# Kernel optimization log

Hardware: AMD Instinct MI355X
Metric: run time of the kernel (lower is better)

The kernel has to match this reference:

```python
import jax, jax.numpy as jnp
import numpy as np

N = 8192      # num nodes (pad index == N, matching the original's 15004 sentinel)
IN = 128; H = 128; OUT = 128
T = 512       # number of teams
L = 30        # max_len
SAMPLE = 5    # sample team size
DCAT = 2 * H + OUT


def _glorot(k, shape):
    lim = np.sqrt(6.0 / (shape[0] + shape[1]))
    return jax.random.uniform(k, shape, jnp.float32, -lim, lim)


def setup_inputs() -> dict:
    key = jax.random.key(0)
    ks = jax.random.split(key, 32)
    x = jax.random.normal(ks[0], (1, N, IN), jnp.float32)
    # sparse-ish binary dense adjacency, avg degree ~16 (memory-bound adj@x)
    adj = (jax.random.uniform(ks[1], (1, N, N), jnp.float32) < 16.0 / N).astype(jnp.float32)
    # team index matrix, ragged lengths in [SAMPLE+1, L], padded with N
    lens = jax.random.randint(ks[2], (T,), SAMPLE + 1, L + 1)
    ids = jax.random.randint(ks[3], (T, L), 0, N)
    teams = jnp.where(jnp.arange(L)[None, :] < lens[:, None], ids, N)
    # DenseGraphConv params: lin_rel (W,b) on adj@x, lin_root (no bias) on x
    p = dict(
        W1r=_glorot(ks[4], (IN, H)), b1=jnp.zeros((H,), jnp.float32), W1s=_glorot(ks[5], (IN, H)),
        W2r=_glorot(ks[6], (H, H)), b2=jnp.zeros((H,), jnp.float32), W2s=_glorot(ks[7], (H, H)),
        W3r=_glorot(ks[8], (H, OUT)), b3=jnp.zeros((OUT,), jnp.float32), W3s=_glorot(ks[9], (H, OUT)),
        g1=jnp.ones((H,), jnp.float32), be1=jnp.zeros((H,), jnp.float32),
        g2=jnp.ones((H,), jnp.float32), be2=jnp.zeros((H,), jnp.float32),
        g3=jnp.ones((OUT,), jnp.float32), be3=jnp.zeros((OUT,), jnp.float32),
        Wl=_glorot(ks[10], (DCAT, OUT)), bl=jnp.zeros((OUT,), jnp.float32),
        att=_glorot(ks[11], (T, L)),  # xavier_uniform'd attention vectors
    )
    return dict(x=x, adj=adj, teams=teams, sample_len=SAMPLE, **p)


def _bn(h, g, b):
    # BatchNorm1d in training mode over flattened (B*N, C), biased variance
    B, n, C = h.shape
    h2 = h.reshape(-1, C)
    mu = h2.mean(0)
    var = h2.var(0)
    return (((h2 - mu) * jax.lax.rsqrt(var + 1e-5)) * g + b).reshape(B, n, C)


def _conv(x, adj, Wr, br, Ws):
    # DenseGraphConv: lin_rel(adj @ x) + lin_root(x)
    return jnp.einsum('bnm,bmf,fo->bno', adj, x, Wr) + br + jnp.einsum('bnf,fo->bno', x, Ws)


def reference(x, adj, teams, sample_len, W1r, b1, W1s, W2r, b2, W2s, W3r, b3, W3s,
              g1, be1, g2, be2, g3, be3, Wl, bl, att):
    x1 = _bn(jax.nn.relu(_conv(x, adj, W1r, b1, W1s)), g1, be1)
    x2 = _bn(jax.nn.relu(_conv(x1, adj, W2r, b2, W2s)), g2, be2)
    x3 = _bn(jax.nn.relu(_conv(x2, adj, W3r, b3, W3s)), g3, be3)
    xcat = jnp.concatenate([x1, x2, x3], axis=-1)               # [1,N,DCAT]
    s = jax.nn.relu(xcat @ Wl + bl)
    appended = jnp.concatenate([xcat[0], jnp.zeros((1, xcat.shape[-1]), xcat.dtype)], 0)  # [N+1,D]
    gathered = appended[teams]                                   # [T,L,D] ragged gather
    # team: full softmax over attention vector (pad positions keep softmax mass,
    # but gather the zero row -> contribute zero, matching the original)
    a_team = jax.nn.softmax(att, axis=-1)
    team_emb = jnp.einsum('tl,tld->td', a_team, gathered)
    pos = jnp.arange(teams.shape[1])[None, :]
    # sample: sub-softmax over the attention entries at the sample members' positions
    m_s = pos < sample_len
    a_s = jax.nn.softmax(jnp.where(m_s, att, -1e30), axis=-1)
    sample_emb = jnp.einsum('tl,tld->td', a_s, gathered)
    # remain: team minus sample minus pad sentinel
    m_r = (pos >= sample_len) & (teams != N)
    a_r = jax.nn.softmax(jnp.where(m_r, att, -1e30), axis=-1)
    remain_emb = jnp.einsum('tl,tld->td', a_r, gathered)
    return s, xcat, team_emb, sample_emb, remain_emb
```

## Files before the change

### kernel.cpp

```cpp
#include <hip/hip_runtime.h>
#include <stdint.h>

#define NN 8192
#define CC 128
#define TT 512
#define LL 30
#define CAP 64

typedef unsigned int uint32;
typedef unsigned short u16;

typedef float f32x4 __attribute__((ext_vector_type(4)));
typedef short bf16x8 __attribute__((ext_vector_type(8)));

__device__ __forceinline__ float bf2f(uint32 h) { return __uint_as_float(h << 16); }
__device__ __forceinline__ u16 f2bf(float f) {
    uint32 u = __float_as_uint(f);
    u = (u + 0x7fffu + ((u >> 16) & 1u)) >> 16;
    return (u16)u;
}
__device__ __forceinline__ uint32 pack2(float a, float b) {
    return (uint32)f2bf(a) | ((uint32)f2bf(b) << 16);
}

__device__ __forceinline__ void stats_reduce(const float* __restrict__ P,
                                             const float* __restrict__ g,
                                             const float* __restrict__ be,
                                             float* __restrict__ coefOut, int tid) {
    __shared__ float SS[256], QQ[256];
    int c = tid & 127, half = tid >> 7;
    float s = 0.f, q = 0.f;
    int b0 = half * 128;
#pragma unroll 8
    for (int b = b0; b < b0 + 128; ++b) {
        s += P[b * 256 + c];
        q += P[b * 256 + 128 + c];
    }
    SS[tid] = s; QQ[tid] = q;
    __syncthreads();
    if (tid < 128) {
        float sum = SS[tid] + SS[tid + 128];
        float sq = QQ[tid] + QQ[tid + 128];
        float mu = sum * (1.f / NN);
        float var = sq * (1.f / NN) - mu * mu;
        float rs = rsqrtf(var + 1e-5f);
        float a = g[tid] * rs;
        coefOut[tid] = a;
        coefOut[128 + tid] = be[tid] - mu * a;
    }
}

__global__ __launch_bounds__(256) void k_pre(
    const float* __restrict__ adj,
    const float* __restrict__ W1r, const float* __restrict__ W1s,
    const float* __restrict__ W2r, const float* __restrict__ W2s,
    const float* __restrict__ W3r, const float* __restrict__ W3s,
    const float* __restrict__ Wl, const float* __restrict__ x0,
    int* __restrict__ nbr, int* __restrict__ cnt,
    u16* __restrict__ wfrag, u16* __restrict__ x0bf,
    u16* __restrict__ yp1, u16* __restrict__ yp2, u16* __restrict__ yp3,
    u16* __restrict__ Abraw, float* __restrict__ coefs) {
    int b = blockIdx.x, tid = threadIdx.x;
    if (b < 2048) {
        int row = b * 4 + (tid >> 6);
        int lane = tid & 63;
        const float4* arow = (const float4*)(adj + (size_t)row * NN);
        int base = 0;
        int* dst = nbr + (size_t)row * CAP;
        for (int it = 0; it < 32; ++it) {
            float4 v = arow[it * 64 + lane];
            float vv[4] = {v.x, v.y, v.z, v.w};
#pragma unroll
            for (int j = 0; j < 4; ++j) {
                unsigned long long m = __ballot(vv[j] != 0.f);
                if (vv[j] != 0.f) {
                    int pos = base + __popcll(m & ((1ull << lane) - 1ull));
                    if (pos < CAP) dst[pos] = it * 256 + lane * 4 + j;
                }
                base += __popcll(m);
            }
        }
        int nn = base < CAP ? base : CAP;
        int npad = (nn + 3) & ~3;
        for (int p = nn + lane; p < npad; p += 64) dst[p] = NN;
        if (lane == 0) cnt[row] = nn;
        int c = lane * 2;
        float a0 = 0.f, a1 = 0.f;
        for (int j = 0; j < npad; j += 4) {
            int4 m = *(const int4*)(dst + j);
            if (m.x < NN) { float2 v = *(const float2*)(x0 + (size_t)m.x * CC + c); a0 += v.x; a1 += v.y; }
            if (m.y < NN) { float2 v = *(const float2*)(x0 + (size_t)m.y * CC + c); a0 += v.x; a1 += v.y; }
            if (m.z < NN) { float2 v = *(const float2*)(x0 + (size_t)m.z * CC + c); a0 += v.x; a1 += v.y; }
            if (m.w < NN) { float2 v = *(const float2*)(x0 + (size_t)m.w * CC + c); a0 += v.x; a1 += v.y; }
        }
        *(uint32*)(Abraw + (size_t)row * CC + c) = pack2(a0, a1);
    } else if (b < 2336) {
        int bb = b - 2048;
        const float* Wa;
        const float* Wb;
        int tile, gbase;
        if (bb < 64)       { Wa = W1r; Wb = W1s; tile = bb;       gbase = 0; }
        else if (bb < 128) { Wa = W2r; Wb = W2s; tile = bb - 64;  gbase = 64; }
        else if (bb < 192) { Wa = W3r; Wb = W3s; tile = bb - 128; gbase = 128; }
        else               { Wa = Wl;  Wb = nullptr; tile = bb - 192; gbase = 192; }
        int kt = tile >> 3, nt = tile & 7;
        int lane = tid & 63, i0 = (tid >> 6) * 2;
        int n = nt * 16 + (lane & 15);
        u16* dst = wfrag + ((size_t)(gbase + tile) * 64 + lane) * 8;
#pragma unroll
        for (int ii = 0; ii < 2; ++ii) {
            int i = i0 + ii;
            int k = kt * 32 + ((lane >> 4) * 8) + i;
            float v;
            if (Wb) v = (k < 128) ? Wa[k * CC + n] : Wb[(k - 128) * CC + n];
            else    v = Wa[k * CC + n];
            dst[i] = f2bf(v);
        }
    } else if (b < 3360) {
        int idx = (b - 2336) * 1024 + tid * 4;
        float4 v = *(const float4*)(x0 + idx);
        ushort4 o;
        o.x = f2bf(v.x); o.y = f2bf(v.y); o.z = f2bf(v.z); o.w = f2bf(v.w);
        *(ushort4*)(x0bf + idx) = o;
    } else {
        if (tid < 128) {
            x0bf[(size_t)NN * CC + tid] = 0;
            yp1[(size_t)NN * CC + tid] = 0;
            yp2[(size_t)NN * CC + tid] = 0;
            yp3[(size_t)NN * CC + tid] = 0;
            coefs[tid] = 1.f;
            coefs[128 + tid] = 0.f;
        }
    }
}

__global__ __launch_bounds__(256) void k_agg(const u16* __restrict__ src,
                                             const int* __restrict__ nbr,
                                             const int* __restrict__ cnt,
                                             u16* __restrict__ Abraw,
                                             const float* __restrict__ P,
                                             const float* __restrict__ g,
                                             const float* __restrict__ be,
                                             float* __restrict__ coefOut) {
    if (blockIdx.x >= 2048) {
        stats_reduce(P, g, be, coefOut, threadIdx.x);
        return;
    }
    int row = blockIdx.x * 4 + (threadIdx.x >> 6);
    int lane = threadIdx.x & 63;
    int c = lane * 2;
    int nreal = cnt[row];
    int npad = (nreal + 3) & ~3;
    const int* nb = nbr + (size_t)row * CAP;
    float a0 = 0.f, a1 = 0.f;
    for (int j = 0; j < npad; j += 4) {
        int4 m = *(const int4*)(nb + j);
        uint32 v0 = *(const uint32*)(src + (size_t)m.x * CC + c);
        uint32 v1 = *(const uint32*)(src + (size_t)m.y * CC + c);
        uint32 v2 = *(const uint32*)(src + (size_t)m.z * CC + c);
        uint32 v3 = *(const uint32*)(src + (size_t)m.w * CC + c);
        a0 += bf2f(v0 & 0xffffu); a1 += bf2f(v0 >> 16);
        a0 += bf2f(v1 & 0xffffu); a1 += bf2f(v1 >> 16);
        a0 += bf2f(v2 & 0xffffu); a1 += bf2f(v2 >> 16);
        a0 += bf2f(v3 & 0xffffu); a1 += bf2f(v3 >> 16);
    }
    *(uint32*)(Abraw + (size_t)row * CC + c) = pack2(a0, a1);
}

__global__ __launch_bounds__(512) void k_gemm(const u16* __restrict__ Abraw,
                                              const u16* __restrict__ yprev,
                                              const int* __restrict__ cnt,
                                              const u16* __restrict__ wfrag,
                                              const float* __restrict__ bias,
                                              const float* __restrict__ coefIn,
                                              u16* __restrict__ yp,
                                              float* __restrict__ partials) {
    __shared__ u16 A[32][264];
    __shared__ float sSum[CC], sSq[CC];
    int tid = threadIdx.x, lane = tid & 63, wid = tid >> 6;
    int row0 = blockIdx.x * 32;
    if (tid < CC) { sSum[tid] = 0.f; sSq[tid] = 0.f; }
    for (int i = tid; i < 1024; i += 512) {
        int r = i >> 5, k = (i & 31) * 8;
        int row = row0 + r;
        uint4 raw;
        float fn;
        int c;
        if (k < 128) {
            c = k;
            raw = *(const uint4*)(Abraw + (size_t)row * CC + k);
            fn = (float)cnt[row];
        } else {
            c = k - 128;
            raw = *(const uint4*)(yprev + (size_t)row * CC + c);
            fn = 1.f;
        }
        float4 a0 = *(const float4*)(coefIn + c);
        float4 a1 = *(const float4*)(coefIn + c + 4);
        float4 b0 = *(const float4*)(coefIn + 128 + c);
        float4 b1 = *(const float4*)(coefIn + 128 + c + 4);
        uint4 o;
        o.x = pack2(a0.x * bf2f(raw.x & 0xffffu) + b0.x * fn, a0.y * bf2f(raw.x >> 16) + b0.y * fn);
        o.y = pack2(a0.z * bf2f(raw.y & 0xffffu) + b0.z * fn, a0.w * bf2f(raw.y >> 16) + b0.w * fn);
        o.z = pack2(a1.x * bf2f(raw.z & 0xffffu) + b1.x * fn, a1.y * bf2f(raw.z >> 16) + b1.y * fn);
        o.w = pack2(a1.z * bf2f(raw.w & 0xffffu) + b1.z * fn, a1.w * bf2f(raw.w >> 16) + b1.w * fn);
        *(uint4*)&A[r][k] = o;
    }
    __syncthreads();

    int mh = wid >> 2, nh = wid & 3;
    int arow = mh * 16 + (lane & 15);
    int kg = (lane >> 4) * 8;
    f32x4 acc[2];
#pragma unroll
    for (int nt = 0; nt < 2; ++nt) acc[nt] = (f32x4){0.f, 0.f, 0.f, 0.f};
#pragma unroll
    for (int kt = 0; kt < 8; ++kt) {
        bf16x8 a = *(const bf16x8*)&A[arow][kt * 32 + kg];
        const u16* wb = wfrag + ((size_t)(kt * 8 + nh * 2) * 64 + lane) * 8;
#pragma unroll
        for (int nt = 0; nt < 2; ++nt) {
            bf16x8 bfr = *(const bf16x8*)(wb + (size_t)nt * 512);
            acc[nt] = __builtin_amdgcn_mfma_f32_16x16x32_bf16(a, bfr, acc[nt], 0, 0, 0);
        }
    }
    int rowb = row0 + mh * 16 + ((lane >> 4) * 4);
#pragma unroll
    for (int nt = 0; nt < 2; ++nt) {
        int col = nh * 32 + nt * 16 + (lane & 15);
        float bv = bias[col];
        float s1 = 0.f, s2 = 0.f;
#pragma unroll
        for (int q = 0; q < 4; ++q) {
            float y = acc[nt][q] + bv;
            y = y > 0.f ? y : 0.f;
            yp[(size_t)(rowb + q) * CC + col] = f2bf(y);
            s1 += y;
            s2 += y * y;
        }
        s1 += __shfl_xor(s1, 16); s1 += __shfl_xor(s1, 32);
        s2 += __shfl_xor(s2, 16); s2 += __shfl_xor(s2, 32);
        if ((lane >> 4) == 0) { atomicAdd(&sSum[col], s1); atomicAdd(&sSq[col], s2); }
    }
    __syncthreads();
    if (tid < CC) {
        partials[(size_t)blockIdx.x * 256 + tid] = sSum[tid];
        partials[(size_t)blockIdx.x * 256 + CC + tid] = sSq[tid];
    }
}

__global__ __launch_bounds__(256) void k_coef3(const float* __restrict__ P,
                                               const float* __restrict__ g,
                                               const float* __restrict__ be,
                                               float* __restrict__ coefOut) {
    stats_reduce(P, g, be, coefOut, threadIdx.x);
}

__global__ __launch_bounds__(256) void k_out(
    const u16* __restrict__ yp1, const u16* __restrict__ yp2, const u16* __restrict__ yp3,
    const float* __restrict__ coefs,
    const u16* __restrict__ wfrag, const float* __restrict__ bias,
    const int* __restrict__ teams, const int* __restrict__ slen_p,
    const float* __restrict__ att,
    float* __restrict__ sout, float* __restrict__ xcat,
    float* __restrict__ oT, float* __restrict__ oS, float* __restrict__ oR) {
    int b = blockIdx.x, tid = threadIdx.x;
    if (b < 512) {
        __shared__ u16 A[16][392];
        int lane = tid & 63, wid = tid >> 6;
        int row0 = b * 16;
        for (int i = tid; i < 768; i += 256) {
            int r = i / 48, kk = (i % 48) * 8;
            int seg = kk >> 7, c = kk & 127;
            const u16* sp = (seg == 0 ? yp1 : seg == 1 ? yp2 : yp3) + (size_t)(row0 + r) * CC + c;
            uint4 raw = *(const uint4*)sp;
            const float* cf = coefs + seg * 256;
            float4 av0 = *(const float4*)(cf + c);
            float4 av1 = *(const float4*)(cf + c + 4);
            float4 bv0 = *(const float4*)(cf + 128 + c);
            float4 bv1 = *(const float4*)(cf + 128 + c + 4);
            uint4 o;
            o.x = pack2(av0.x * bf2f(raw.x & 0xffffu) + bv0.x, av0.y * bf2f(raw.x >> 16) + bv0.y);
            o.y = pack2(av0.z * bf2f(raw.y & 0xffffu) + bv0.z, av0.w * bf2f(raw.y >> 16) + bv0.w);
            o.z = pack2(av1.x * bf2f(raw.z & 0xffffu) + bv1.x, av1.y * bf2f(raw.z >> 16) + bv1.y);
            o.w = pack2(av1.z * bf2f(raw.w & 0xffffu) + bv1.z, av1.w * bf2f(raw.w >> 16) + bv1.w);
            *(uint4*)&A[r][kk] = o;
        }
        __syncthreads();
        int nh = wid;
        int arow = lane & 15;
        int kg = (lane >> 4) * 8;
        f32x4 acc[2];
#pragma unroll
        for (int nt = 0; nt < 2; ++nt) acc[nt] = (f32x4){0.f, 0.f, 0.f, 0.f};
#pragma unroll
        for (int kt = 0; kt < 12; ++kt) {
            bf16x8 a = *(const bf16x8*)&A[arow][kt * 32 + kg];
            const u16* wb = wfrag + ((size_t)(kt * 8 + nh * 2) * 64 + lane) * 8;
#pragma unroll
            for (int nt = 0; nt < 2; ++nt) {
                bf16x8 bfr = *(const bf16x8*)(wb + (size_t)nt * 512);
                acc[nt] = __builtin_amdgcn_mfma_f32_16x16x32_bf16(a, bfr, acc[nt], 0, 0, 0);
            }
        }
        int rowb = row0 + ((lane >> 4) * 4);
#pragma unroll
        for (int nt = 0; nt < 2; ++nt) {
            int col = nh * 32 + nt * 16 + (lane & 15);
            float bv = bias[col];
#pragma unroll
            for (int q = 0; q < 4; ++q) {
                float y = acc[nt][q] + bv;
                sout[(size_t)(rowb + q) * CC + col] = y > 0.f ? y : 0.f;
            }
        }
    } else if (b < 1024) {
        __shared__ float wT[LL], wS[LL], wR[LL];
        __shared__ int ids[LL];
        int t = b - 512;
        if (tid < 64) {
            int lane = tid;
            bool act = lane < LL;
            float a = act ? att[t * LL + lane] : 0.f;
            int id = act ? teams[t * LL + lane] : NN;
            if (act) ids[lane] = id;
            int sl = *slen_p;
            const float NEG = -1e30f;
            float v = act ? a : NEG;
#pragma unroll
            for (int o = 32; o > 0; o >>= 1) v = fmaxf(v, __shfl_xor(v, o));
            float mT = v;
            float eT = act ? __expf(a - mT) : 0.f;
            v = eT;
#pragma unroll
            for (int o = 32; o > 0; o >>= 1) v += __shfl_xor(v, o);
            float sT = v;
            bool inS = act && (lane < sl);
            v = inS ? a : NEG;
#pragma unroll
            for (int o = 32; o > 0; o >>= 1) v = fmaxf(v, __shfl_xor(v, o));
            float mS = v;
            float eS = inS ? __expf(a - mS) : 0.f;
            v = eS;
#pragma unroll
            for (int o = 32; o > 0; o >>= 1) v += __shfl_xor(v, o);
            float sS = v;
            bool inR = act && (lane >= sl) && (id != NN);
            v = inR ? a : NEG;
#pragma unroll
            for (int o = 32; o > 0; o >>= 1) v = fmaxf(v, __shfl_xor(v, o));
            float mR = v;
            float eR = inR ? __expf(a - mR) : 0.f;
            v = eR;
#pragma unroll
            for (int o = 32; o > 0; o >>= 1) v += __shfl_xor(v, o);
            float sR = v;
            if (act) {
                wT[lane] = eT / sT;
                wS[lane] = eS / sS;
                wR[lane] = eR / sR;
            }
        }
        __syncthreads();
        for (int d = tid; d < 384; d += 256) {
            int seg = d >> 7, c = d & 127;
            const u16* xb = seg == 0 ? yp1 : seg == 1 ? yp2 : yp3;
            float ca = coefs[seg * 256 + c];
            float cb = coefs[seg * 256 + 128 + c];
            float aT = 0.f, aS = 0.f, aR = 0.f;
            for (int l = 0; l < LL; ++l) {
                int id = ids[l];
                if (id < NN) {
                    float vv = ca * bf2f((uint32)xb[(size_t)id * CC + c]) + cb;
                    aT += wT[l] * vv;
                    aS += wS[l] * vv;
                    aR += wR[l] * vv;
                }
            }
            oT[(size_t)t * 384 + d] = aT;
            oS[(size_t)t * 384 + d] = aS;
            oR[(size_t)t * 384 + d] = aR;
        }
    } else {
        int idx = (b - 1024) * 256 + tid;
        int n = idx / 96;
        int k = (idx % 96) * 4;
        int seg = k >> 7, c = k & 127;
        const u16* sp = (seg == 0 ? yp1 : seg == 1 ? yp2 : yp3) + (size_t)n * CC + c;
        ushort4 raw = *(const ushort4*)sp;
        const float* cf = coefs + seg * 256;
        float4 a = *(const float4*)(cf + c);
        float4 bb = *(const float4*)(cf + 128 + c);
        float4 o;
        o.x = a.x * bf2f((uint32)raw.x) + bb.x;
        o.y = a.y * bf2f((uint32)raw.y) + bb.y;
        o.z = a.z * bf2f((uint32)raw.z) + bb.z;
        o.w = a.w * bf2f((uint32)raw.w) + bb.w;
        *(float4*)(xcat + (size_t)n * 384 + k) = o;
    }
}

extern "C" void kernel_launch(void* const* d_in, const int* in_sizes, int n_in,
                              void* d_out, int out_size, void* d_ws, size_t ws_size,
                              hipStream_t stream) {
    const float* x = (const float*)d_in[0];
    const float* adj = (const float*)d_in[1];
    const int* teams = (const int*)d_in[2];
    const int* slen = (const int*)d_in[3];
    const float* W1r = (const float*)d_in[4];
    const float* b1 = (const float*)d_in[5];
    const float* W1s = (const float*)d_in[6];
    const float* W2r = (const float*)d_in[7];
    const float* b2 = (const float*)d_in[8];
    const float* W2s = (const float*)d_in[9];
    const float* W3r = (const float*)d_in[10];
    const float* b3 = (const float*)d_in[11];
    const float* W3s = (const float*)d_in[12];
    const float* g1 = (const float*)d_in[13];
    const float* be1 = (const float*)d_in[14];
    const float* g2 = (const float*)d_in[15];
    const float* be2 = (const float*)d_in[16];
    const float* g3 = (const float*)d_in[17];
    const float* be3 = (const float*)d_in[18];
    const float* Wl = (const float*)d_in[19];
    const float* bl = (const float*)d_in[20];
    const float* att = (const float*)d_in[21];

    float* out = (float*)d_out;
    float* s_out = out;
    float* xcat = out + (size_t)NN * CC;
    float* oT = xcat + (size_t)NN * 384;
    float* oS = oT + (size_t)TT * 384;
    float* oR = oS + (size_t)TT * 384;

    char* ws = (char*)d_ws;
    size_t off = 0;
    int* nbr = (int*)(ws + off); off += (size_t)NN * CAP * 4;
    int* cnt = (int*)(ws + off); off += (size_t)NN * 4;
    u16* x0bf = (u16*)(ws + off); off += (size_t)(NN + 1) * CC * 2;
    u16* yp1 = (u16*)(ws + off); off += (size_t)(NN + 1) * CC * 2;
    u16* yp2 = (u16*)(ws + off); off += (size_t)(NN + 1) * CC * 2;
    u16* yp3 = (u16*)(ws + off); off += (size_t)(NN + 1) * CC * 2;
    u16* Abraw = (u16*)(ws + off); off += (size_t)NN * CC * 2;
    u16* wfrag = (u16*)(ws + off); off += (size_t)288 * 512 * 2;
    float* partials = (float*)(ws + off); off += (size_t)256 * 256 * 4;
    float* coefs = (float*)(ws + off); off += (size_t)4 * 256 * 4;

    k_pre<<<3361, 256, 0, stream>>>(adj, W1r, W1s, W2r, W2s, W3r, W3s, Wl, x,
                                    nbr, cnt, wfrag, x0bf, yp1, yp2, yp3, Abraw, coefs);
    k_gemm<<<256, 512, 0, stream>>>(Abraw, x0bf, cnt, wfrag, b1, coefs, yp1, partials);
    k_agg<<<2049, 256, 0, stream>>>(yp1, nbr, cnt, Abraw, partials, g1, be1, coefs + 256);
    k_gemm<<<256, 512, 0, stream>>>(Abraw, yp1, cnt, wfrag + 64 * 512, b2, coefs + 256, yp2, partials);
    k_agg<<<2049, 256, 0, stream>>>(yp2, nbr, cnt, Abraw, partials, g2, be2, coefs + 512);
    k_gemm<<<256, 512, 0, stream>>>(Abraw, yp2, cnt, wfrag + 128 * 512, b3, coefs + 512, yp3, partials);
    k_coef3<<<1, 256, 0, stream>>>(partials, g3, be3, coefs + 768);
    k_out<<<4096, 256, 0, stream>>>(yp1, yp2, yp3, coefs + 256,
                                    wfrag + 192 * 512, bl, teams, slen, att,
                                    s_out, xcat, oT, oS, oR);
}
```

Baseline: 129.7 us.

## Accumulate BatchNorm stats with fixed-point atomics and drop separate reduce kernel

Each GEMM block now adds its per-column sum and sum-of-squares into a global 64-bit fixed-point accumulator with integer atomics. This replaces the per-block partials array and the extra reduction block in k_agg, and removes the separate k_coef3 launch. Consumer kernels (the next GEMM and k_out) recompute the BN scale and shift from the accumulated stats in shared memory. The layer-1 GEMM converts x to bf16 inline, so the x0bf conversion pass and its buffer are gone. The costs are atomic contention on 256 addresses, redundant coefficient recomputation in every k_out block, and fixed-point quantization of the stats.

Result: no change. 131.4 us (+1.3%).

```diff
diff --git a/kernel.cpp b/kernel.cpp
--- a/kernel.cpp
+++ b/kernel.cpp
@@ -8,10 +8,14 @@
 #define CAP 64
 
 typedef unsigned int uint32;
+typedef unsigned long long ull;
 typedef unsigned short u16;
 
 typedef float f32x4 __attribute__((ext_vector_type(4)));
 typedef short bf16x8 __attribute__((ext_vector_type(8)));
+
+#define STAT_SCALE 1048576.0f
+#define STAT_INV (1.0f / 1048576.0f)
 
 __device__ __forceinline__ float bf2f(uint32 h) { return __uint_as_float(h << 16); }
 __device__ __forceinline__ u16 f2bf(float f) {
@@ -22,32 +26,17 @@
 __device__ __forceinline__ uint32 pack2(float a, float b) {
     return (uint32)f2bf(a) | ((uint32)f2bf(b) << 16);
 }
-
-__device__ __forceinline__ void stats_reduce(const float* __restrict__ P,
-                                             const float* __restrict__ g,
-                                             const float* __restrict__ be,
-                                             float* __restrict__ coefOut, int tid) {
-    __shared__ float SS[256], QQ[256];
-    int c = tid & 127, half = tid >> 7;
-    float s = 0.f, q = 0.f;
-    int b0 = half * 128;
-#pragma unroll 8
-    for (int b = b0; b < b0 + 128; ++b) {
-        s += P[b * 256 + c];
-        q += P[b * 256 + 128 + c];
-    }
-    SS[tid] = s; QQ[tid] = q;
-    __syncthreads();
-    if (tid < 128) {
-        float sum = SS[tid] + SS[tid + 128];
-        float sq = QQ[tid] + QQ[tid + 128];
-        float mu = sum * (1.f / NN);
-        float var = sq * (1.f / NN) - mu * mu;
-        float rs = rsqrtf(var + 1e-5f);
-        float a = g[tid] * rs;
-        coefOut[tid] = a;
-        coefOut[128 + tid] = be[tid] - mu * a;
-    }
+__device__ __forceinline__ void coef_from_stats(const ull* __restrict__ st, int c,
+                                                const float* __restrict__ g,
+                                                const float* __restrict__ be,
+                                                float& ca, float& cb) {
+    float s = (float)(long long)st[c] * STAT_INV;
+    float q = (float)(long long)st[128 + c] * STAT_INV;
+    float mu = s * (1.f / NN);
+    float var = q * (1.f / NN) - mu * mu;
+    float rs = rsqrtf(var + 1e-5f);
+    ca = g[c] * rs;
+    cb = be[c] - mu * ca;
 }
 
 __global__ __launch_bounds__(256) void k_pre(
@@ -57,9 +46,9 @@
     const float* __restrict__ W3r, const float* __restrict__ W3s,
     const float* __restrict__ Wl, const float* __restrict__ x0,
     int* __restrict__ nbr, int* __restrict__ cnt,
-    u16* __restrict__ wfrag, u16* __restrict__ x0bf,
+    u16* __restrict__ wfrag,
     u16* __restrict__ yp1, u16* __restrict__ yp2, u16* __restrict__ yp3,
-    u16* __restrict__ Abraw, float* __restrict__ coefs) {
+    u16* __restrict__ Abraw, ull* __restrict__ statsAcc) {
     int b = blockIdx.x, tid = threadIdx.x;
     if (b < 2048) {
         int row = b * 4 + (tid >> 6);
@@ -116,20 +105,16 @@
             else    v = Wa[k * CC + n];
             dst[i] = f2bf(v);
         }
-    } else if (b < 3360) {
-        int idx = (b - 2336) * 1024 + tid * 4;
-        float4 v = *(const float4*)(x0 + idx);
-        ushort4 o;
-        o.x = f2bf(v.x); o.y = f2bf(v.y); o.z = f2bf(v.z); o.w = f2bf(v.w);
-        *(ushort4*)(x0bf + idx) = o;
     } else {
         if (tid < 128) {
-            x0bf[(size_t)NN * CC + tid] = 0;
             yp1[(size_t)NN * CC + tid] = 0;
             yp2[(size_t)NN * CC + tid] = 0;
             yp3[(size_t)NN * CC + tid] = 0;
-            coefs[tid] = 1.f;
-            coefs[128 + tid] = 0.f;
+#pragma unroll
+            for (int l = 0; l < 3; ++l) {
+                statsAcc[l * 256 + tid] = 0ull;
+                statsAcc[l * 256 + 128 + tid] = 0ull;
+            }
         }
     }
 }
@@ -137,15 +122,7 @@
 __global__ __launch_bounds__(256) void k_agg(const u16* __restrict__ src,
                                              const int* __restrict__ nbr,
                                              const int* __restrict__ cnt,
-                                             u16* __restrict__ Abraw,
-                                             const float* __restrict__ P,
-                                             const float* __restrict__ g,
-                                             const float* __restrict__ be,
-                                             float* __restrict__ coefOut) {
-    if (blockIdx.x >= 2048) {
-        stats_reduce(P, g, be, coefOut, threadIdx.x);
-        return;
-    }
+                                             u16* __restrict__ Abraw) {
     int row = blockIdx.x * 4 + (threadIdx.x >> 6);
     int lane = threadIdx.x & 63;
     int c = lane * 2;
@@ -167,43 +144,69 @@
     *(uint32*)(Abraw + (size_t)row * CC + c) = pack2(a0, a1);
 }
 
+template <int LAYER>
 __global__ __launch_bounds__(512) void k_gemm(const u16* __restrict__ Abraw,
+                                              const float* __restrict__ x0,
                                               const u16* __restrict__ yprev,
                                               const int* __restrict__ cnt,
                                               const u16* __restrict__ wfrag,
                                               const float* __restrict__ bias,
-                                              const float* __restrict__ coefIn,
-                                              u16* __restrict__ yp,
-                                              float* __restrict__ partials) {
+                                              const ull* __restrict__ statsPrev,
+                                              const float* __restrict__ g,
+                                              const float* __restrict__ be,
+                                              ull* __restrict__ statsOut,
+                                              u16* __restrict__ yp) {
     __shared__ u16 A[32][264];
     __shared__ float sSum[CC], sSq[CC];
+    __shared__ alignas(16) float cA[CC];
+    __shared__ alignas(16) float cB[CC];
     int tid = threadIdx.x, lane = tid & 63, wid = tid >> 6;
     int row0 = blockIdx.x * 32;
-    if (tid < CC) { sSum[tid] = 0.f; sSq[tid] = 0.f; }
+    if (tid < CC) {
+        sSum[tid] = 0.f; sSq[tid] = 0.f;
+        if constexpr (LAYER > 1) {
+            float a, b;
+            coef_from_stats(statsPrev, tid, g, be, a, b);
+            cA[tid] = a; cB[tid] = b;
+        }
+    }
+    __syncthreads();
     for (int i = tid; i < 1024; i += 512) {
         int r = i >> 5, k = (i & 31) * 8;
         int row = row0 + r;
-        uint4 raw;
-        float fn;
-        int c;
-        if (k < 128) {
-            c = k;
-            raw = *(const uint4*)(Abraw + (size_t)row * CC + k);
-            fn = (float)cnt[row];
+        uint4 o;
+        if constexpr (LAYER == 1) {
+            if (k < 128) {
+                o = *(const uint4*)(Abraw + (size_t)row * CC + k);
+            } else {
+                int c = k - 128;
+                float4 v0 = *(const float4*)(x0 + (size_t)row * CC + c);
+                float4 v1 = *(const float4*)(x0 + (size_t)row * CC + c + 4);
+                o.x = pack2(v0.x, v0.y); o.y = pack2(v0.z, v0.w);
+                o.z = pack2(v1.x, v1.y); o.w = pack2(v1.z, v1.w);
+            }
         } else {
-            c = k - 128;
-            raw = *(const uint4*)(yprev + (size_t)row * CC + c);
-            fn = 1.f;
-        }
-        float4 a0 = *(const float4*)(coefIn + c);
-        float4 a1 = *(const float4*)(coefIn + c + 4);
-        float4 b0 = *(const float4*)(coefIn + 128 + c);
-        float4 b1 = *(const float4*)(coefIn + 128 + c + 4);
-        uint4 o;
-        o.x = pack2(a0.x * bf2f(raw.x & 0xffffu) + b0.x * fn, a0.y * bf2f(raw.x >> 16) + b0.y * fn);
-        o.y = pack2(a0.z * bf2f(raw.y & 0xffffu) + b0.z * fn, a0.w * bf2f(raw.y >> 16) + b0.w * fn);
-        o.z = pack2(a1.x * bf2f(raw.z & 0xffffu) + b1.x * fn, a1.y * bf2f(raw.z >> 16) + b1.y * fn);
-        o.w = pack2(a1.z * bf2f(raw.w & 0xffffu) + b1.z * fn, a1.w * bf2f(raw.w >> 16) + b1.w * fn);
+            uint4 raw;
+            float fn;
+            int c;
+            if (k < 128) {
+                c = k;
+                raw = *(const uint4*)(Abraw + (size_t)row * CC + k);
+                fn = (float)cnt[row];
+            } else {
+                c = k - 128;
+                raw = *(const uint4*)(yprev + (size_t)row * CC + c);
+                fn = 1.f;
+            }
+            float4 a0 = *(const float4*)(cA + c);
+            float4 a1 = *(const float4*)(cA + c + 4);
+            float4 b0 = *(const float4*)(cB + c);
+            float4 b1 = *(const float4*)(cB + c + 4);
+            o.x = pack2(a0.x * bf2f(raw.x & 0xffffu) + b0.x * fn, a0.y * bf2f(raw.x >> 16) + b0.y * fn);
+            o.y = pack2(a0.z * bf2f(raw.y & 0xffffu) + b0.z * fn, a0.w * bf2f(raw.y >> 16) + b0.w * fn);
+            o.z = pack2(a1.x * bf2f(raw.z & 0xffffu) + b1.x * fn, a1.y * bf2f(raw.z >> 16) + b1.y * fn);
+            o.w = pack2(a1.z * bf2f(raw.w & 0xffffu) + b1.z * fn, a1.w * bf2f(raw.w >> 16) + b1.w * fn);
+        }
         *(uint4*)&A[r][k] = o;
     }
     __syncthreads();
@@ -243,38 +246,49 @@
         if ((lane >> 4) == 0) { atomicAdd(&sSum[col], s1); atomicAdd(&sSq[col], s2); }
     }
     __syncthreads();
-    if (tid < CC) {
-        partials[(size_t)blockIdx.x * 256 + tid] = sSum[tid];
-        partials[(size_t)blockIdx.x * 256 + CC + tid] = sSq[tid];
-    }
-}
-
-__global__ __launch_bounds__(256) void k_coef3(const float* __restrict__ P,
-                                               const float* __restrict__ g,
-                                               const float* __restrict__ be,
-                                               float* __restrict__ coefOut) {
-    stats_reduce(P, g, be, coefOut, threadIdx.x);
+    if (tid < 128) {
+        atomicAdd(statsOut + tid, (ull)(long long)llrintf(sSum[tid] * STAT_SCALE));
+    } else if (tid < 256) {
+        atomicAdd(statsOut + tid, (ull)(long long)llrintf(sSq[tid - 128] * STAT_SCALE));
+    }
 }
 
 __global__ __launch_bounds__(256) void k_out(
     const u16* __restrict__ yp1, const u16* __restrict__ yp2, const u16* __restrict__ yp3,
-    const float* __restrict__ coefs,
-    const u16* __restrict__ wfrag, const float* __restrict__ bias,
+    const ull* __restrict__ statsAcc,
+    const float* __restrict__ g1, const float* __restrict__ be1,
+    const float* __restrict__ g2, const float* __restrict__ be2,
+    const float* __restrict__ g3, const float* __restrict__ be3,
+    const u16* __restrict__ wfL, const float* __restrict__ bias,
     const int* __restrict__ teams, const int* __restrict__ slen_p,
     const float* __restrict__ att,
     float* __restrict__ sout, float* __restrict__ xcat,
     float* __restrict__ oT, float* __restrict__ oS, float* __restrict__ oR) {
+    __shared__ alignas(16) char pool[12544];
+    __shared__ alignas(16) float cAll[768];
     int b = blockIdx.x, tid = threadIdx.x;
+    if (tid < 128) {
+        const float* gs[3] = {g1, g2, g3};
+        const float* bes[3] = {be1, be2, be3};
+#pragma unroll
+        for (int l = 0; l < 3; ++l) {
+            float a, bb;
+            coef_from_stats(statsAcc + l * 256, tid, gs[l], bes[l], a, bb);
+            cAll[l * 256 + tid] = a;
+            cAll[l * 256 + 128 + tid] = bb;
+        }
+    }
+    __syncthreads();
+    const u16* yps[3] = {yp1, yp2, yp3};
     if (b < 512) {
-        __shared__ u16 A[16][392];
+        u16 (*A)[392] = (u16(*)[392])pool;
         int lane = tid & 63, wid = tid >> 6;
         int row0 = b * 16;
         for (int i = tid; i < 768; i += 256) {
             int r = i / 48, kk = (i % 48) * 8;
             int seg = kk >> 7, c = kk & 127;
-            const u16* sp = (seg == 0 ? yp1 : seg == 1 ? yp2 : yp3) + (size_t)(row0 + r) * CC + c;
-            uint4 raw = *(const uint4*)sp;
-            const float* cf = coefs + seg * 256;
+            uint4 raw = *(const uint4*)(yps[seg] + (size_t)(row0 + r) * CC + c);
+            const float* cf = cAll + seg * 256;
             float4 av0 = *(const float4*)(cf + c);
             float4 av1 = *(const float4*)(cf + c + 4);
             float4 bv0 = *(const float4*)(cf + 128 + c);
@@ -296,7 +310,7 @@
 #pragma unroll
         for (int kt = 0; kt < 12; ++kt) {
             bf16x8 a = *(const bf16x8*)&A[arow][kt * 32 + kg];
-            const u16* wb = wfrag + ((size_t)(kt * 8 + nh * 2) * 64 + lane) * 8;
+            const u16* wb = wfL + ((size_t)(kt * 8 + nh * 2) * 64 + lane) * 8;
 #pragma unroll
             for (int nt = 0; nt < 2; ++nt) {
                 bf16x8 bfr = *(const bf16x8*)(wb + (size_t)nt * 512);
@@ -315,8 +329,10 @@
             }
         }
     } else if (b < 1024) {
-        __shared__ float wT[LL], wS[LL], wR[LL];
-        __shared__ int ids[LL];
+        float* wT = (float*)pool;
+        float* wS = wT + 32;
+        float* wR = wS + 32;
+        int* ids = (int*)(wR + 32);
         int t = b - 512;
         if (tid < 64) {
             int lane = tid;
@@ -364,9 +380,9 @@
         __syncthreads();
         for (int d = tid; d < 384; d += 256) {
             int seg = d >> 7, c = d & 127;
-            const u16* xb = seg == 0 ? yp1 : seg == 1 ? yp2 : yp3;
-            float ca = coefs[seg * 256 + c];
-            float cb = coefs[seg * 256 + 128 + c];
+            const u16* xb = yps[seg];
+            float ca = cAll[seg * 256 + c];
+            float cb = cAll[seg * 256 + 128 + c];
             float aT = 0.f, aS = 0.f, aR = 0.f;
             for (int l = 0; l < LL; ++l) {
                 int id = ids[l];
@@ -386,9 +402,8 @@
         int n = idx / 96;
         int k = (idx % 96) * 4;
         int seg = k >> 7, c = k & 127;
-        const u16* sp = (seg == 0 ? yp1 : seg == 1 ? yp2 : yp3) + (size_t)n * CC + c;
-        ushort4 raw = *(const ushort4*)sp;
-        const float* cf = coefs + seg * 256;
+        ushort4 raw = *(const ushort4*)(yps[seg] + (size_t)n * CC + c);
+        const float* cf = cAll + seg * 256;
         float4 a = *(const float4*)(cf + c);
         float4 bb = *(const float4*)(cf + 128 + c);
         float4 o;
@@ -437,24 +452,25 @@
     size_t off = 0;
     int* nbr = (int*)(ws + off); off += (size_t)NN * CAP * 4;
     int* cnt = (int*)(ws + off); off += (size_t)NN * 4;
-    u16* x0bf = (u16*)(ws + off); off += (size_t)(NN + 1) * CC * 2;
     u16* yp1 = (u16*)(ws + off); off += (size_t)(NN + 1) * CC * 2;
     u16* yp2 = (u16*)(ws + off); off += (size_t)(NN + 1) * CC * 2;
     u16* yp3 = (u16*)(ws + off); off += (size_t)(NN + 1) * CC * 2;
     u16* Abraw = (u16*)(ws + off); off += (size_t)NN * CC * 2;
     u16* wfrag = (u16*)(ws + off); off += (size_t)288 * 512 * 2;
-    float* partials = (float*)(ws + off); off += (size_t)256 * 256 * 4;
-    float* coefs = (float*)(ws + off); off += (size_t)4 * 256 * 4;
-
-    k_pre<<<3361, 256, 0, stream>>>(adj, W1r, W1s, W2r, W2s, W3r, W3s, Wl, x,
-                                    nbr, cnt, wfrag, x0bf, yp1, yp2, yp3, Abraw, coefs);
-    k_gemm<<<256, 512, 0, stream>>>(Abraw, x0bf, cnt, wfrag, b1, coefs, yp1, partials);
-    k_agg<<<2049, 256, 0, stream>>>(yp1, nbr, cnt, Abraw, partials, g1, be1, coefs + 256);
-    k_gemm<<<256, 512, 0, stream>>>(Abraw, yp1, cnt, wfrag + 64 * 512, b2, coefs + 256, yp2, partials);
-    k_agg<<<2049, 256, 0, stream>>>(yp2, nbr, cnt, Abraw, partials, g2, be2, coefs + 512);
-    k_gemm<<<256, 512, 0, stream>>>(Abraw, yp2, cnt, wfrag + 128 * 512, b3, coefs + 512, yp3, partials);
-    k_coef3<<<1, 256, 0, stream>>>(partials, g3, be3, coefs + 768);
-    k_out<<<4096, 256, 0, stream>>>(yp1, yp2, yp3, coefs + 256,
+    ull* statsAcc = (ull*)(ws + off); off += (size_t)768 * 8;
+
+    k_pre<<<2337, 256, 0, stream>>>(adj, W1r, W1s, W2r, W2s, W3r, W3s, Wl, x,
+                                    nbr, cnt, wfrag, yp1, yp2, yp3, Abraw, statsAcc);
+    k_gemm<1><<<256, 512, 0, stream>>>(Abraw, x, nullptr, cnt, wfrag, b1,
+                                       nullptr, nullptr, nullptr, statsAcc, yp1);
+    k_agg<<<2048, 256, 0, stream>>>(yp1, nbr, cnt, Abraw);
+    k_gemm<2><<<256, 512, 0, stream>>>(Abraw, nullptr, yp1, cnt, wfrag + 64 * 512, b2,
+                                       statsAcc, g1, be1, statsAcc + 256, yp2);
+    k_agg<<<2048, 256, 0, stream>>>(yp2, nbr, cnt, Abraw);
+    k_gemm<3><<<256, 512, 0, stream>>>(Abraw, nullptr, yp2, cnt, wfrag + 128 * 512, b3,
+                                       statsAcc + 256, g2, be2, statsAcc + 512, yp3);
+    k_out<<<4096, 256, 0, stream>>>(yp1, yp2, yp3, statsAcc,
+                                    g1, be1, g2, be2, g3, be3,
                                     wfrag + 192 * 512, bl, teams, slen, att,
                                     s_out, xcat, oT, oS, oR);
 }
```
